# Kernel tuning notes

Measured on AMD Instinct MI355X. Metric: run time of the kernel, lower is better.

The kernel has to match this reference:

```python
import jax, jax.numpy as jnp
import numpy as np

D_MODEL = 512
N_HEADS = 8
D_HEAD = 64
D_FF = 1024
EPS = 1e-5


def setup_inputs() -> dict:
    key = jax.random.key(0)
    ks = jax.random.split(key, 9)
    B, L = 4, 2048
    s = lambda fan_in: 1.0 / np.sqrt(fan_in)
    return {
        "x": jax.random.normal(ks[0], (B, L, D_MODEL), dtype=jnp.float32),
        "ln1_w": jnp.ones((D_MODEL,), jnp.float32),
        "ln1_b": jnp.zeros((D_MODEL,), jnp.float32),
        "ln2_w": jnp.ones((D_MODEL,), jnp.float32),
        "ln2_b": jnp.zeros((D_MODEL,), jnp.float32),
        "wq": jax.random.normal(ks[1], (D_MODEL, N_HEADS * D_HEAD), jnp.float32) * s(D_MODEL),
        "wk": jax.random.normal(ks[2], (D_MODEL, N_HEADS * D_HEAD), jnp.float32) * s(D_MODEL),
        "wv": jax.random.normal(ks[3], (D_MODEL, N_HEADS * D_HEAD), jnp.float32) * s(D_MODEL),
        "wo": jax.random.normal(ks[4], (N_HEADS * D_HEAD, D_MODEL), jnp.float32) * s(N_HEADS * D_HEAD),
        "w_gate": jax.random.normal(ks[5], (D_MODEL, D_FF), jnp.float32) * s(D_MODEL),
        "w_up": jax.random.normal(ks[6], (D_MODEL, D_FF), jnp.float32) * s(D_MODEL),
        "w_down": jax.random.normal(ks[7], (D_FF, D_MODEL), jnp.float32) * s(D_FF),
    }


def _layernorm(x, w, b):
    mu = jnp.mean(x, axis=-1, keepdims=True)
    var = jnp.var(x, axis=-1, keepdims=True)
    return (x - mu) * jax.lax.rsqrt(var + EPS) * w + b


def reference(x, ln1_w, ln1_b, ln2_w, ln2_b, wq, wk, wv, wo, w_gate, w_up, w_down):
    B, L, _ = x.shape
    scale = D_HEAD ** -0.5

    # --- attention sublayer (pre-LN residual) ---
    h = _layernorm(x, ln1_w, ln1_b)
    q = (h @ wq).reshape(B, L, N_HEADS, D_HEAD)  # [B,L,H,Dh]
    k = (h @ wk).reshape(B, L, N_HEADS, D_HEAD)
    v = (h @ wv).reshape(B, L, N_HEADS, D_HEAD)
    scores = jnp.einsum("bqhd,bkhd->bhqk", q, k) * scale
    # softmax computed in fp32, cast back (matches F.softmax(dtype=float32).to(q.dtype))
    attn = jax.nn.softmax(scores.astype(jnp.float32), axis=-1).astype(q.dtype)
    out = jnp.einsum("bhqk,bkhd->bqhd", attn, v).reshape(B, L, N_HEADS * D_HEAD)
    x = x + out @ wo

    # --- SwiGLU FFN sublayer (pre-LN residual) ---
    h = _layernorm(x, ln2_w, ln2_b)
    gate = jax.nn.silu(h @ w_gate)
    x = x + (gate * (h @ w_up)) @ w_down
    return x
```

## Files before the change

### kernel.cpp

```cpp
#include <hip/hip_runtime.h>
#include <hip/hip_bf16.h>
#include <math.h>

#define EPS 1e-5f

typedef __attribute__((ext_vector_type(8))) short bf16x8;
typedef __attribute__((ext_vector_type(4))) float f32x4;
typedef __attribute__((ext_vector_type(16))) float f32x16;

#define MFMA16 __builtin_amdgcn_mfma_f32_16x16x32_bf16
#define MFMA32 __builtin_amdgcn_mfma_f32_32x32x16_bf16

__device__ __forceinline__ short f2bf(float x) {
    union { float f; unsigned u; } un; un.f = x;
    unsigned r = un.u + 0x7FFF + ((un.u >> 16) & 1);
    return (short)(r >> 16);
}
__device__ __forceinline__ float bf2f(short s) {
    union { unsigned u; float f; } un;
    un.u = ((unsigned)(unsigned short)s) << 16;
    return un.f;
}
__device__ __forceinline__ unsigned pack_bf2(float a, float b) {
    unsigned r;
    asm("v_cvt_pk_bf16_f32 %0, %1, %2" : "=v"(r) : "v"(a), "v"(b));
    return r;
}
__device__ __forceinline__ float exp2_fast(float x) {
    float r;
    asm("v_exp_f32 %0, %1" : "=v"(r) : "v"(x));
    return r;
}
__device__ __forceinline__ void permswap(unsigned& a, unsigned& b) {
    asm volatile("v_permlane32_swap_b32 %0, %1" : "+v"(a), "+v"(b));
}
__device__ __forceinline__ bf16x8 mk_frag(unsigned a, unsigned b, unsigned c, unsigned d) {
    union { unsigned u[4]; bf16x8 v; } t;
    t.u[0] = a; t.u[1] = b; t.u[2] = c; t.u[3] = d;
    return t.v;
}
__device__ __forceinline__ void load_lds16(const short* g, short* l) {
    __builtin_amdgcn_global_load_lds(
        (const __attribute__((address_space(1))) unsigned int*)g,
        (__attribute__((address_space(3))) unsigned int*)l, 16, 0, 0);
}
__device__ __forceinline__ void wait_vm0_barrier() {
    asm volatile("s_waitcnt vmcnt(0)" ::: "memory");
    __builtin_amdgcn_s_barrier();
    __builtin_amdgcn_sched_barrier(0);
}

__global__ __launch_bounds__(256) void ln_kernel_b(const float* __restrict__ in,
                                                   const float* __restrict__ w,
                                                   const float* __restrict__ bb,
                                                   short* __restrict__ out) {
    int wv = threadIdx.x >> 6, lane = threadIdx.x & 63;
    int row = blockIdx.x * 4 + wv;
    const float* x = in + (size_t)row * 512 + lane * 8;
    float4 v0 = *(const float4*)x;
    float4 v1 = *(const float4*)(x + 4);
    float s  = (v0.x + v0.y) + (v0.z + v0.w) + (v1.x + v1.y) + (v1.z + v1.w);
    float s2 = v0.x*v0.x + v0.y*v0.y + v0.z*v0.z + v0.w*v0.w
             + v1.x*v1.x + v1.y*v1.y + v1.z*v1.z + v1.w*v1.w;
#pragma unroll
    for (int off = 1; off < 64; off <<= 1) {
        s  += __shfl_xor(s, off);
        s2 += __shfl_xor(s2, off);
    }
    float mu = s * (1.f / 512.f);
    float rstd = rsqrtf(s2 * (1.f / 512.f) - mu * mu + EPS);
    const float4 wa = *(const float4*)&w[lane * 8];
    const float4 wb = *(const float4*)&w[lane * 8 + 4];
    const float4 ba = *(const float4*)&bb[lane * 8];
    const float4 bv = *(const float4*)&bb[lane * 8 + 4];
    uint4 o;
    o.x = pack_bf2((v0.x - mu) * rstd * wa.x + ba.x, (v0.y - mu) * rstd * wa.y + ba.y);
    o.y = pack_bf2((v0.z - mu) * rstd * wa.z + ba.z, (v0.w - mu) * rstd * wa.w + ba.w);
    o.z = pack_bf2((v1.x - mu) * rstd * wb.x + bv.x, (v1.y - mu) * rstd * wb.y + bv.y);
    o.w = pack_bf2((v1.z - mu) * rstd * wb.z + bv.z, (v1.w - mu) * rstd * wb.w + bv.w);
    *(uint4*)&out[(size_t)row * 512 + lane * 8] = o;
}

struct WT { const float* w; short* t; int K; int N; };
struct WT7 { WT a[7]; };
__global__ __launch_bounds__(256) void transp_w_kernel(WT7 p) {
    WT e = p.a[blockIdx.z];
    int k0 = blockIdx.x * 32, n0 = blockIdx.y * 32;
    if (k0 >= e.K || n0 >= e.N) return;
    __shared__ short t[32][33];
    int tx = threadIdx.x & 31, ty = threadIdx.x >> 5;
#pragma unroll
    for (int pp = 0; pp < 4; pp++)
        t[pp * 8 + ty][tx] = f2bf(e.w[(size_t)(k0 + pp * 8 + ty) * e.N + n0 + tx]);
    __syncthreads();
#pragma unroll
    for (int pp = 0; pp < 4; pp++)
        e.t[(size_t)(n0 + pp * 8 + ty) * e.K + k0 + tx] = t[tx][pp * 8 + ty];
}

template <int EPI, int BM, int BN>
__global__ __launch_bounds__(256) void gemm_mfma(const short* __restrict__ A,
                                                 const short* __restrict__ Bt,
                                                 const float* __restrict__ res,
                                                 void* __restrict__ Cv,
                                                 int M, int N, int K) {
    constexpr int MI = BM >> 5;
    constexpr int NJ = BN >> 5;
    __shared__ short As[2][BM * 64];
    __shared__ short Bs[2][BN * 64];
    const int tid = threadIdx.x;
    const int lane = tid & 63, w = tid >> 6;
    const int g = lane >> 4, r16 = lane & 15;
    const int wr = w >> 1, wc = w & 1;

    const int nb = gridDim.x * gridDim.y;
    const int fid = blockIdx.y * gridDim.x + blockIdx.x;
    const int nid = (fid & 7) * (nb >> 3) + (fid >> 3);
    const int m0 = (nid / gridDim.x) * BM, n0 = (nid % gridDim.x) * BN;

    const int lr = lane >> 3;
    const int ck = (lane & 7) ^ lr;

    auto stage = [&](int buf, int k0) {
#pragma unroll
        for (int p = 0; p < BM / 32; p++) {
            int rb = w * (BM / 4) + p * 8;
            load_lds16(&A[(size_t)(m0 + rb + lr) * K + k0 + ck * 8], &As[buf][rb * 64]);
        }
#pragma unroll
        for (int p = 0; p < BN / 32; p++) {
            int rb = w * (BN / 4) + p * 8;
            load_lds16(&Bt[(size_t)(n0 + rb + lr) * K + k0 + ck * 8], &Bs[buf][rb * 64]);
        }
    };

    f32x4 acc[MI][NJ] = {};
    stage(0, 0);
    wait_vm0_barrier();

    const int nt = K >> 6;
    int cur = 0;
    for (int t = 0; t < nt; t++) {
        if (t + 1 < nt) stage(cur ^ 1, (t + 1) << 6);
#pragma unroll
        for (int ks = 0; ks < 2; ks++) {
            bf16x8 av[MI], bv[NJ];
#pragma unroll
            for (int i = 0; i < MI; i++) {
                int row = wr * (BM >> 1) + i * 16 + r16;
                av[i] = *(const bf16x8*)&As[cur][row * 64 + ((ks * 4 + g) ^ (row & 7)) * 8];
            }
#pragma unroll
            for (int j = 0; j < NJ; j++) {
                int row = wc * (BN >> 1) + j * 16 + r16;
                bv[j] = *(const bf16x8*)&Bs[cur][row * 64 + ((ks * 4 + g) ^ (row & 7)) * 8];
            }
#pragma unroll
            for (int i = 0; i < MI; i++)
#pragma unroll
                for (int j = 0; j < NJ; j++)
                    acc[i][j] = MFMA16(av[i], bv[j], acc[i][j], 0, 0, 0);
        }
        wait_vm0_barrier();
        cur ^= 1;
    }

#pragma unroll
    for (int i = 0; i < MI; i++)
#pragma unroll
        for (int j = 0; j < NJ; j++)
#pragma unroll
            for (int jr = 0; jr < 4; jr++) {
                int m = m0 + wr * (BM >> 1) + i * 16 + 4 * g + jr;
                int n = n0 + wc * (BN >> 1) + j * 16 + r16;
                float v = acc[i][j][jr];
                if (EPI == 0) {
                    size_t idx = (size_t)m * N + n;
                    ((float*)Cv)[idx] = res[idx] + v;
                } else {
                    if (n < 512) v *= 0.18033688011112042f;
                    ((short*)Cv)[(size_t)(n >> 9) * 4194304 +
                                 (((size_t)(m >> 11) * 8 + ((n >> 6) & 7)) * 2048 + (m & 2047)) * 64 + (n & 63)] = f2bf(v);
                }
            }
}

__global__ __launch_bounds__(256) void ffn_gateup_kernel(const short* __restrict__ A,
                                                         const short* __restrict__ Bg,
                                                         const short* __restrict__ Bu,
                                                         short* __restrict__ U,
                                                         int M, int N, int K) {
    constexpr int BM = 128, BN = 64;
    constexpr int MI = 4, NJ = 2;
    __shared__ short As[2][BM * 64];
    __shared__ short Bgs[2][BN * 64];
    __shared__ short Bus[2][BN * 64];
    const int tid = threadIdx.x;
    const int lane = tid & 63, w = tid >> 6;
    const int g = lane >> 4, r16 = lane & 15;
    const int wr = w >> 1, wc = w & 1;

    const int nb = gridDim.x * gridDim.y;
    const int fid = blockIdx.y * gridDim.x + blockIdx.x;
    const int nid = (fid & 7) * (nb >> 3) + (fid >> 3);
    const int m0 = (nid / gridDim.x) * BM, n0 = (nid % gridDim.x) * BN;

    const int lr = lane >> 3;
    const int ck = (lane & 7) ^ lr;

    auto stage = [&](int buf, int k0) {
#pragma unroll
        for (int p = 0; p < 4; p++) {
            int rb = w * 32 + p * 8;
            load_lds16(&A[(size_t)(m0 + rb + lr) * K + k0 + ck * 8], &As[buf][rb * 64]);
        }
#pragma unroll
        for (int p = 0; p < 2; p++) {
            int rb = w * 16 + p * 8;
            load_lds16(&Bg[(size_t)(n0 + rb + lr) * K + k0 + ck * 8], &Bgs[buf][rb * 64]);
            load_lds16(&Bu[(size_t)(n0 + rb + lr) * K + k0 + ck * 8], &Bus[buf][rb * 64]);
        }
    };

    f32x4 accg[MI][NJ] = {};
    f32x4 accu[MI][NJ] = {};
    stage(0, 0);
    wait_vm0_barrier();

    const int nt = K >> 6;
    int cur = 0;
    for (int t = 0; t < nt; t++) {
        if (t + 1 < nt) stage(cur ^ 1, (t + 1) << 6);
#pragma unroll
        for (int ks = 0; ks < 2; ks++) {
            bf16x8 av[MI], bgv[NJ], buv[NJ];
#pragma unroll
            for (int i = 0; i < MI; i++) {
                int row = wr * 64 + i * 16 + r16;
                av[i] = *(const bf16x8*)&As[cur][row * 64 + ((ks * 4 + g) ^ (row & 7)) * 8];
            }
#pragma unroll
            for (int j = 0; j < NJ; j++) {
                int row = wc * 32 + j * 16 + r16;
                int off = row * 64 + ((ks * 4 + g) ^ (row & 7)) * 8;
                bgv[j] = *(const bf16x8*)&Bgs[cur][off];
                buv[j] = *(const bf16x8*)&Bus[cur][off];
            }
#pragma unroll
            for (int i = 0; i < MI; i++)
#pragma unroll
                for (int j = 0; j < NJ; j++) {
                    accg[i][j] = MFMA16(av[i], bgv[j], accg[i][j], 0, 0, 0);
                    accu[i][j] = MFMA16(av[i], buv[j], accu[i][j], 0, 0, 0);
                }
        }
        wait_vm0_barrier();
        cur ^= 1;
    }

#pragma unroll
    for (int i = 0; i < MI; i++)
#pragma unroll
        for (int j = 0; j < NJ; j++)
#pragma unroll
            for (int jr = 0; jr < 4; jr++) {
                int m = m0 + wr * 64 + i * 16 + 4 * g + jr;
                int n = n0 + wc * 32 + j * 16 + r16;
                float gt = accg[i][j][jr];
                float y = gt / (1.f + __expf(-gt)) * accu[i][j][jr];
                U[(size_t)m * N + n] = f2bf(y);
            }
}

__global__ __launch_bounds__(256) void transp_v_kernel(const short* __restrict__ vb,
                                                       short* __restrict__ vt) {
    __shared__ short tile[64][65];
    int l0 = blockIdx.x * 64;
    int bh = blockIdx.y;
    const size_t base = (size_t)bh * 2048 * 64;
    int tid = threadIdx.x;
#pragma unroll
    for (int p = 0; p < 4; p++) {
        int r = p * 16 + (tid >> 4);
        int c4 = (tid & 15) * 4;
        *(short4*)&tile[r][c4] = *(const short4*)&vb[base + (size_t)(l0 + r) * 64 + c4];
    }
    __syncthreads();
#pragma unroll
    for (int p = 0; p < 4; p++) {
        int d = p * 16 + (tid >> 4);
        int c4 = (tid & 15) * 4;
        short4 o;
        o.x = tile[c4 + 0][d]; o.y = tile[c4 + 1][d];
        o.z = tile[c4 + 2][d]; o.w = tile[c4 + 3][d];
        *(short4*)&vt[base + (size_t)d * 2048 + l0 + c4] = o;
    }
}

__global__ __launch_bounds__(256) void attn_mfma_kernel(const short* __restrict__ qb,
                                                        const short* __restrict__ kb,
                                                        const short* __restrict__ vt,
                                                        short* __restrict__ outb) {
    __shared__ short SM[16384];

    const int fid = blockIdx.y * gridDim.x + blockIdx.x;
    const int nid = (fid & 7) * 64 + (fid >> 3);
    const int bh = nid >> 4, qt = nid & 15;
    const int b = bh >> 3, h = bh & 7;
    const int q0 = qt * 128;
    const size_t hb = (size_t)bh * (2048 * 64);

    const int tid = threadIdx.x;
    const int lane = tid & 63, w = tid >> 6;
    const int hi = lane >> 5;
    const int l31 = lane & 31;
    const int lr = lane >> 3, ck = (lane & 7) ^ lr;

#pragma unroll
    for (int p = 0; p < 4; p++)
        load_lds16(&qb[hb + (size_t)(q0 + 32 * w + 8 * p + lr) * 64 + ck * 8],
                   &SM[8192 + (32 * w + 8 * p) * 64]);
    wait_vm0_barrier();
    bf16x8 qf[4];
    {
        int row = 32 * w + l31;
#pragma unroll
        for (int ds = 0; ds < 4; ds++)
            qf[ds] = *(const bf16x8*)&SM[8192 + row * 64 + ((2 * ds + hi) ^ (row & 7)) * 8];
    }
    asm volatile("s_waitcnt lgkmcnt(0)" ::: "memory");
    __builtin_amdgcn_s_barrier();
    __builtin_amdgcn_sched_barrier(0);

    auto stageKV = [&](int buf, int kt) {
        int k0 = kt * 64;
        int rb = w * 16;
        short* Kd = &SM[buf * 4096];
        short* Vd = &SM[8192 + buf * 4096];
        load_lds16(&kb[hb + (size_t)(k0 + rb + lr) * 64 + ck * 8],       &Kd[rb * 64]);
        load_lds16(&kb[hb + (size_t)(k0 + rb + 8 + lr) * 64 + ck * 8],   &Kd[(rb + 8) * 64]);
        load_lds16(&vt[hb + (size_t)(rb + lr) * 2048 + k0 + ck * 8],     &Vd[rb * 64]);
        load_lds16(&vt[hb + (size_t)(rb + 8 + lr) * 2048 + k0 + ck * 8], &Vd[(rb + 8) * 64]);
    };
    stageKV(0, 0);
    wait_vm0_barrier();

    float m_ = -1e30f, l_ = 0.f;
    f32x16 o0 = (f32x16)(0.f), o1 = (f32x16)(0.f);
    int cur = 0;

    for (int t = 0; t < 32; t++) {
        if (t + 1 < 32) stageKV(cur ^ 1, t + 1);
        const short* Kc = &SM[cur * 4096];
        const short* Vc = &SM[8192 + cur * 4096];

        f32x16 s0 = (f32x16)(0.f), s1 = (f32x16)(0.f);
        {
            int r0 = l31, r1 = 32 + l31;
            int cshift = (l31 & 7);
#pragma unroll
            for (int ds = 0; ds < 4; ds++) {
                bf16x8 k0f = *(const bf16x8*)&Kc[r0 * 64 + ((2 * ds + hi) ^ cshift) * 8];
                bf16x8 k1f = *(const bf16x8*)&Kc[r1 * 64 + ((2 * ds + hi) ^ cshift) * 8];
                s0 = MFMA32(k0f, qf[ds], s0, 0, 0, 0);
                s1 = MFMA32(k1f, qf[ds], s1, 0, 0, 0);
            }
        }

        float q0m = fmaxf(fmaxf(s0[0], s0[1]),  fmaxf(s0[2], s0[3]));
        float q1m = fmaxf(fmaxf(s0[4], s0[5]),  fmaxf(s0[6], s0[7]));
        float q2m = fmaxf(fmaxf(s0[8], s0[9]),  fmaxf(s0[10], s0[11]));
        float q3m = fmaxf(fmaxf(s0[12], s0[13]), fmaxf(s0[14], s0[15]));
        float q4m = fmaxf(fmaxf(s1[0], s1[1]),  fmaxf(s1[2], s1[3]));
        float q5m = fmaxf(fmaxf(s1[4], s1[5]),  fmaxf(s1[6], s1[7]));
        float q6m = fmaxf(fmaxf(s1[8], s1[9]),  fmaxf(s1[10], s1[11]));
        float q7m = fmaxf(fmaxf(s1[12], s1[13]), fmaxf(s1[14], s1[15]));
        float om = fmaxf(fmaxf(fmaxf(q0m, q1m), fmaxf(q2m, q3m)),
                         fmaxf(fmaxf(q4m, q5m), fmaxf(q6m, q7m)));
        unsigned ua = __float_as_uint(om), ub = ua;
        permswap(ua, ub);
        float pm = fmaxf(__uint_as_float(ua), __uint_as_float(ub));

        if (!__all(pm - m_ <= 8.f)) {
            float mn = fmaxf(m_, pm);
            float al = exp2_fast(m_ - mn);
            l_ *= al;
            o0 *= al;
            o1 *= al;
            m_ = mn;
        }

        float rs = 0.f;
#pragma unroll
        for (int r = 0; r < 16; r++) { s0[r] = exp2_fast(s0[r] - m_); rs += s0[r]; }
#pragma unroll
        for (int r = 0; r < 16; r++) { s1[r] = exp2_fast(s1[r] - m_); rs += s1[r]; }
        l_ += rs;

        bf16x8 pf[4];
#pragma unroll
        for (int ks = 0; ks < 2; ks++) {
            unsigned X0 = pack_bf2(s0[8 * ks + 0], s0[8 * ks + 1]);
            unsigned X1 = pack_bf2(s0[8 * ks + 2], s0[8 * ks + 3]);
            unsigned Y0 = pack_bf2(s0[8 * ks + 4], s0[8 * ks + 5]);
            unsigned Y1 = pack_bf2(s0[8 * ks + 6], s0[8 * ks + 7]);
            permswap(X0, Y0);
            permswap(X1, Y1);
            pf[ks] = mk_frag(X0, X1, Y0, Y1);
        }
#pragma unroll
        for (int ks = 0; ks < 2; ks++) {
            unsigned X0 = pack_bf2(s1[8 * ks + 0], s1[8 * ks + 1]);
            unsigned X1 = pack_bf2(s1[8 * ks + 2], s1[8 * ks + 3]);
            unsigned Y0 = pack_bf2(s1[8 * ks + 4], s1[8 * ks + 5]);
            unsigned Y1 = pack_bf2(s1[8 * ks + 6], s1[8 * ks + 7]);
            permswap(X0, Y0);
            permswap(X1, Y1);
            pf[2 + ks] = mk_frag(X0, X1, Y0, Y1);
        }

        {
            int r0 = l31, r1 = 32 + l31;
            int cs0 = r0 & 7, cs1 = r1 & 7;
#pragma unroll
            for (int kk = 0; kk < 4; kk++) {
                int kc = 2 * kk + hi;
                bf16x8 v0f = *(const bf16x8*)&Vc[r0 * 64 + (kc ^ cs0) * 8];
                bf16x8 v1f = *(const bf16x8*)&Vc[r1 * 64 + (kc ^ cs1) * 8];
                o0 = MFMA32(v0f, pf[kk], o0, 0, 0, 0);
                o1 = MFMA32(v1f, pf[kk], o1, 0, 0, 0);
            }
        }

        wait_vm0_barrier();
        cur ^= 1;
    }

    unsigned sa = __float_as_uint(l_), sb = sa;
    permswap(sa, sb);
    float inv = 1.f / (__uint_as_float(sa) + __uint_as_float(sb));
    int q = q0 + 32 * w + l31;
    size_t obase = ((size_t)b * 2048 + q) * 512 + h * 64;
#pragma unroll
    for (int rr = 0; rr < 4; rr++) {
        int d0 = 8 * rr + 4 * hi;
        unsigned long long pv =
            (unsigned long long)pack_bf2(o0[4 * rr + 0] * inv, o0[4 * rr + 1] * inv)
          | ((unsigned long long)pack_bf2(o0[4 * rr + 2] * inv, o0[4 * rr + 3] * inv) << 32);
        *(unsigned long long*)&outb[obase + d0] = pv;
        unsigned long long pv2 =
            (unsigned long long)pack_bf2(o1[4 * rr + 0] * inv, o1[4 * rr + 1] * inv)
          | ((unsigned long long)pack_bf2(o1[4 * rr + 2] * inv, o1[4 * rr + 3] * inv) << 32);
        *(unsigned long long*)&outb[obase + 32 + d0] = pv2;
    }
}

extern "C" void kernel_launch(void* const* d_in, const int* in_sizes, int n_in,
                              void* d_out, int out_size, void* d_ws, size_t ws_size,
                              hipStream_t stream) {
    const float* x      = (const float*)d_in[0];
    const float* ln1_w  = (const float*)d_in[1];
    const float* ln1_b  = (const float*)d_in[2];
    const float* ln2_w  = (const float*)d_in[3];
    const float* ln2_b  = (const float*)d_in[4];
    const float* wq     = (const float*)d_in[5];
    const float* wk     = (const float*)d_in[6];
    const float* wv     = (const float*)d_in[7];
    const float* wo     = (const float*)d_in[8];
    const float* w_gate = (const float*)d_in[9];
    const float* w_up   = (const float*)d_in[10];
    const float* w_down = (const float*)d_in[11];
    float* out = (float*)d_out;

    const int M = 4 * 2048;
    char* ws = (char*)d_ws;
    const size_t MB = 1 << 20;
    short* h1b   = (short*)(ws);
    short* qb    = (short*)(ws + 8 * MB);
    short* kb    = (short*)(ws + 16 * MB);
    short* vb    = (short*)(ws + 24 * MB);
    short* vt    = (short*)(ws + 32 * MB);
    short* aob   = (short*)(ws + 40 * MB);
    short* u_b   = (short*)(ws + 48 * MB);
    short* qkvT  = (short*)(ws + 80 * MB);
    short* woT   = (short*)(ws + 82 * MB);
    short* wguT  = (short*)(ws + 83 * MB);
    short* wdT   = (short*)(ws + 85 * MB);
    short* h2b   = qb;

    WT7 wt;
    wt.a[0] = {wq,     qkvT,               512,  512};
    wt.a[1] = {wk,     qkvT + 512 * 512,   512,  512};
    wt.a[2] = {wv,     qkvT + 1024 * 512,  512,  512};
    wt.a[3] = {wo,     woT,                512,  512};
    wt.a[4] = {w_gate, wguT,               512, 1024};
    wt.a[5] = {w_up,   wguT + 1024 * 512,  512, 1024};
    wt.a[6] = {w_down, wdT,               1024,  512};

    transp_w_kernel<<<dim3(32, 32, 7), 256, 0, stream>>>(wt);
    ln_kernel_b<<<M / 4, 256, 0, stream>>>(x, ln1_w, ln1_b, h1b);
    gemm_mfma<2, 128, 128><<<dim3(12, 64), 256, 0, stream>>>(h1b, qkvT, nullptr, qb, M, 1536, 512);
    transp_v_kernel<<<dim3(32, 32), 256, 0, stream>>>(vb, vt);
    attn_mfma_kernel<<<dim3(16, 32), 256, 0, stream>>>(qb, kb, vt, aob);
    gemm_mfma<0, 128, 64><<<dim3(8, 64), 256, 0, stream>>>(aob, woT, x, out, M, 512, 512);
    ln_kernel_b<<<M / 4, 256, 0, stream>>>(out, ln2_w, ln2_b, h2b);
    ffn_gateup_kernel<<<dim3(16, 64), 256, 0, stream>>>(h2b, wguT, wguT + 1024 * 512, u_b, M, 1024, 512);
    gemm_mfma<0, 128, 64><<<dim3(8, 64), 256, 0, stream>>>(u_b, wdT, out, out, M, 512, 1024);
}
```

Measured before the change: 155.8 us.

## Fuse LN1 with weight transpose and write V transposed from QKV GEMM

Combines the first layernorm and the weight transpose/convert into one launch, with a flattened block index that avoids the empty blocks of the old 3D grid. The QKV GEMM epilogue now writes V directly in the [d][L] transposed layout, which removes the separate V transpose kernel and its extra read and write. The trade-off is that V stores are strided along m, so they coalesce poorly, and there are two fewer launches.

```diff
diff --git a/kernel.cpp b/kernel.cpp
--- a/kernel.cpp
+++ b/kernel.cpp
@@ -48,6 +48,63 @@
     asm volatile("s_waitcnt vmcnt(0)" ::: "memory");
     __builtin_amdgcn_s_barrier();
     __builtin_amdgcn_sched_barrier(0);
+}
+
+struct WT { const float* w; short* t; int K; int N; };
+struct WT7 { WT a[7]; };
+__global__ __launch_bounds__(256) void prep_kernel(const float* __restrict__ in,
+                                                   const float* __restrict__ lw,
+                                                   const float* __restrict__ lb,
+                                                   short* __restrict__ lo,
+                                                   WT7 p) {
+    __shared__ short t[32][33];
+    int bid = blockIdx.x;
+    if (bid < 2048) {
+        int wv = threadIdx.x >> 6, lane = threadIdx.x & 63;
+        int row = bid * 4 + wv;
+        const float* x = in + (size_t)row * 512 + lane * 8;
+        float4 v0 = *(const float4*)x;
+        float4 v1 = *(const float4*)(x + 4);
+        float s  = (v0.x + v0.y) + (v0.z + v0.w) + (v1.x + v1.y) + (v1.z + v1.w);
+        float s2 = v0.x*v0.x + v0.y*v0.y + v0.z*v0.z + v0.w*v0.w
+                 + v1.x*v1.x + v1.y*v1.y + v1.z*v1.z + v1.w*v1.w;
+#pragma unroll
+        for (int off = 1; off < 64; off <<= 1) {
+            s  += __shfl_xor(s, off);
+            s2 += __shfl_xor(s2, off);
+        }
+        float mu = s * (1.f / 512.f);
+        float rstd = rsqrtf(s2 * (1.f / 512.f) - mu * mu + EPS);
+        const float4 wa = *(const float4*)&lw[lane * 8];
+        const float4 wb = *(const float4*)&lw[lane * 8 + 4];
+        const float4 ba = *(const float4*)&lb[lane * 8];
+        const float4 bv = *(const float4*)&lb[lane * 8 + 4];
+        uint4 o;
+        o.x = pack_bf2((v0.x - mu) * rstd * wa.x + ba.x, (v0.y - mu) * rstd * wa.y + ba.y);
+        o.y = pack_bf2((v0.z - mu) * rstd * wa.z + ba.z, (v0.w - mu) * rstd * wa.w + ba.w);
+        o.z = pack_bf2((v1.x - mu) * rstd * wb.x + bv.x, (v1.y - mu) * rstd * wb.y + bv.y);
+        o.w = pack_bf2((v1.z - mu) * rstd * wb.z + bv.z, (v1.w - mu) * rstd * wb.w + bv.w);
+        *(uint4*)&lo[(size_t)row * 512 + lane * 8] = o;
+    } else {
+        int ti = bid - 2048;
+        int e_idx, base;
+        if (ti < 1024)      { e_idx = ti >> 8; base = e_idx << 8; }
+        else if (ti < 1536) { e_idx = 4; base = 1024; }
+        else if (ti < 2048) { e_idx = 5; base = 1536; }
+        else                { e_idx = 6; base = 2048; }
+        WT e = p.a[e_idx];
+        int lt = ti - base;
+        int nk = e.K >> 5;
+        int k0 = (lt % nk) * 32, n0 = (lt / nk) * 32;
+        int tx = threadIdx.x & 31, ty = threadIdx.x >> 5;
+#pragma unroll
+        for (int pp = 0; pp < 4; pp++)
+            t[pp * 8 + ty][tx] = f2bf(e.w[(size_t)(k0 + pp * 8 + ty) * e.N + n0 + tx]);
+        __syncthreads();
+#pragma unroll
+        for (int pp = 0; pp < 4; pp++)
+            e.t[(size_t)(n0 + pp * 8 + ty) * e.K + k0 + tx] = t[tx][pp * 8 + ty];
+    }
 }
 
 __global__ __launch_bounds__(256) void ln_kernel_b(const float* __restrict__ in,
@@ -79,23 +136,6 @@
     o.z = pack_bf2((v1.x - mu) * rstd * wb.x + bv.x, (v1.y - mu) * rstd * wb.y + bv.y);
     o.w = pack_bf2((v1.z - mu) * rstd * wb.z + bv.z, (v1.w - mu) * rstd * wb.w + bv.w);
     *(uint4*)&out[(size_t)row * 512 + lane * 8] = o;
-}
-
-struct WT { const float* w; short* t; int K; int N; };
-struct WT7 { WT a[7]; };
-__global__ __launch_bounds__(256) void transp_w_kernel(WT7 p) {
-    WT e = p.a[blockIdx.z];
-    int k0 = blockIdx.x * 32, n0 = blockIdx.y * 32;
-    if (k0 >= e.K || n0 >= e.N) return;
-    __shared__ short t[32][33];
-    int tx = threadIdx.x & 31, ty = threadIdx.x >> 5;
-#pragma unroll
-    for (int pp = 0; pp < 4; pp++)
-        t[pp * 8 + ty][tx] = f2bf(e.w[(size_t)(k0 + pp * 8 + ty) * e.N + n0 + tx]);
-    __syncthreads();
-#pragma unroll
-    for (int pp = 0; pp < 4; pp++)
-        e.t[(size_t)(n0 + pp * 8 + ty) * e.K + k0 + tx] = t[tx][pp * 8 + ty];
 }
 
 template <int EPI, int BM, int BN>
@@ -179,8 +219,13 @@
                     ((float*)Cv)[idx] = res[idx] + v;
                 } else {
                     if (n < 512) v *= 0.18033688011112042f;
-                    ((short*)Cv)[(size_t)(n >> 9) * 4194304 +
-                                 (((size_t)(m >> 11) * 8 + ((n >> 6) & 7)) * 2048 + (m & 2047)) * 64 + (n & 63)] = f2bf(v);
+                    if (n < 1024) {
+                        ((short*)Cv)[(size_t)(n >> 9) * 4194304 +
+                                     (((size_t)(m >> 11) * 8 + ((n >> 6) & 7)) * 2048 + (m & 2047)) * 64 + (n & 63)] = f2bf(v);
+                    } else {
+                        ((short*)Cv)[(size_t)2 * 4194304 +
+                                     (((size_t)(m >> 11) * 8 + ((n >> 6) & 7)) * 64 + (n & 63)) * 2048 + (m & 2047)] = f2bf(v);
+                    }
                 }
             }
 }
@@ -270,31 +315,6 @@
                 float y = gt / (1.f + __expf(-gt)) * accu[i][j][jr];
                 U[(size_t)m * N + n] = f2bf(y);
             }
-}
-
-__global__ __launch_bounds__(256) void transp_v_kernel(const short* __restrict__ vb,
-                                                       short* __restrict__ vt) {
-    __shared__ short tile[64][65];
-    int l0 = blockIdx.x * 64;
-    int bh = blockIdx.y;
-    const size_t base = (size_t)bh * 2048 * 64;
-    int tid = threadIdx.x;
-#pragma unroll
-    for (int p = 0; p < 4; p++) {
-        int r = p * 16 + (tid >> 4);
-        int c4 = (tid & 15) * 4;
-        *(short4*)&tile[r][c4] = *(const short4*)&vb[base + (size_t)(l0 + r) * 64 + c4];
-    }
-    __syncthreads();
-#pragma unroll
-    for (int p = 0; p < 4; p++) {
-        int d = p * 16 + (tid >> 4);
-        int c4 = (tid & 15) * 4;
-        short4 o;
-        o.x = tile[c4 + 0][d]; o.y = tile[c4 + 1][d];
-        o.z = tile[c4 + 2][d]; o.w = tile[c4 + 3][d];
-        *(short4*)&vt[base + (size_t)d * 2048 + l0 + c4] = o;
-    }
 }
 
 __global__ __launch_bounds__(256) void attn_mfma_kernel(const short* __restrict__ qb,
@@ -478,8 +498,7 @@
     short* h1b   = (short*)(ws);
     short* qb    = (short*)(ws + 8 * MB);
     short* kb    = (short*)(ws + 16 * MB);
-    short* vb    = (short*)(ws + 24 * MB);
-    short* vt    = (short*)(ws + 32 * MB);
+    short* vt    = (short*)(ws + 24 * MB);
     short* aob   = (short*)(ws + 40 * MB);
     short* u_b   = (short*)(ws + 48 * MB);
     short* qkvT  = (short*)(ws + 80 * MB);
@@ -497,10 +516,8 @@
     wt.a[5] = {w_up,   wguT + 1024 * 512,  512, 1024};
     wt.a[6] = {w_down, wdT,               1024,  512};
 
-    transp_w_kernel<<<dim3(32, 32, 7), 256, 0, stream>>>(wt);
-    ln_kernel_b<<<M / 4, 256, 0, stream>>>(x, ln1_w, ln1_b, h1b);
+    prep_kernel<<<4608, 256, 0, stream>>>(x, ln1_w, ln1_b, h1b, wt);
     gemm_mfma<2, 128, 128><<<dim3(12, 64), 256, 0, stream>>>(h1b, qkvT, nullptr, qb, M, 1536, 512);
-    transp_v_kernel<<<dim3(32, 32), 256, 0, stream>>>(vb, vt);
     attn_mfma_kernel<<<dim3(16, 32), 256, 0, stream>>>(qb, kb, vt, aob);
     gemm_mfma<0, 128, 64><<<dim3(8, 64), 256, 0, stream>>>(aob, woT, x, out, M, 512, 512);
     ln_kernel_b<<<M / 4, 256, 0, stream>>>(out, ln2_w, ln2_b, h2b);
```

After: 160.9 us. 1.03x slower.
